# Kernel optimization log

Measured on AMD Instinct MI355X. Metric: run time of the kernel, lower is better.

Reference implementation:

```python
import jax, jax.numpy as jnp
import numpy as np

B, T, D, DH, DFF = 4, 2048, 1024, 1024, 4096


def setup_inputs() -> dict:
    key = jax.random.key(0)
    ks = jax.random.split(key, 8)
    s = 0.02
    return {
        "x": jax.random.normal(ks[0], (B, T, D), jnp.float32),
        "ln1_g": jnp.ones((D,), jnp.float32),
        "ln1_b": jnp.zeros((D,), jnp.float32),
        "W_q": jax.random.normal(ks[1], (D, DH), jnp.float32) * s,
        "b_q": jnp.zeros((DH,), jnp.float32),
        "W_k": jax.random.normal(ks[2], (D, DH), jnp.float32) * s,
        "b_k": jnp.zeros((DH,), jnp.float32),
        "W_v": jax.random.normal(ks[3], (D, DH), jnp.float32) * s,
        "b_v": jnp.zeros((DH,), jnp.float32),
        "ln2_g": jnp.ones((D,), jnp.float32),
        "ln2_b": jnp.zeros((D,), jnp.float32),
        "W_in": jax.random.normal(ks[4], (D, DFF), jnp.float32) * s,
        "b_in": jnp.zeros((DFF,), jnp.float32),
        "W_out": jax.random.normal(ks[5], (DFF, D), jnp.float32) * s,
        "b_out": jnp.zeros((D,), jnp.float32),
    }


def _layernorm(x, g, b, eps=1e-5):
    mu = jnp.mean(x, axis=-1, keepdims=True)
    var = jnp.var(x, axis=-1, keepdims=True)
    return (x - mu) * jax.lax.rsqrt(var + eps) * g + b


def reference(x, ln1_g, ln1_b, W_q, b_q, W_k, b_k, W_v, b_v,
              ln2_g, ln2_b, W_in, b_in, W_out, b_out):
    # --- attention branch (pre-LN) ---
    h = _layernorm(x, ln1_g, ln1_b)                      # [B,T,D]
    Q = h @ W_q + b_q                                    # [B,T,DH]
    K = h @ W_k + b_k
    V = h @ W_v + b_v
    scale = 1.0 / jnp.sqrt(jnp.asarray(K.shape[-1], h.dtype))
    att = jnp.einsum("btd,bsd->bts", Q, K) * scale       # [B,T,T]
    # NOTE: source calls att.masked_fill(...) without assignment -> mask
    # is discarded; faithfully no causal mask applied here.
    att = jax.nn.softmax(att, axis=-1)
    attn_out = jnp.einsum("bts,bsd->btd", att, V)        # [B,T,DH]
    x = x + attn_out
    # --- MLP branch (pre-LN) ---
    h2 = _layernorm(x, ln2_g, ln2_b)
    ff = jax.nn.gelu(h2 @ W_in + b_in, approximate=False)
    x = x + (ff @ W_out + b_out)
    return x
```

## Files before the change

kernel.cpp:

```cpp
#include <hip/hip_runtime.h>
#include <hip/hip_bf16.h>

#define B_    4
#define T_    2048
#define D_    1024
#define DH_   1024
#define DFF_  4096
#define MTOT  (B_ * T_)

using f32x4  = __attribute__((ext_vector_type(4))) float;
using bf16x8 = __attribute__((ext_vector_type(8))) short;

__device__ __forceinline__ unsigned short f2bf(float f) {
    unsigned u = __builtin_bit_cast(unsigned, f);
    u += 0x7fffu + ((u >> 16) & 1u);
    return (unsigned short)(u >> 16);
}
__device__ __forceinline__ float bf2f(unsigned short h) {
    unsigned u = ((unsigned)h) << 16;
    return __builtin_bit_cast(float, u);
}

__device__ __forceinline__ void gload16(const short* g, short* l) {
    __builtin_amdgcn_global_load_lds(
        (const __attribute__((address_space(1))) unsigned int*)g,
        (__attribute__((address_space(3))) unsigned int*)l, 16, 0, 0);
}

__global__ __launch_bounds__(256) void transp_f32_bf16(
    const float* __restrict__ src, short* __restrict__ dst, int K, int N) {
    __shared__ float tile[32][33];
    int tk = blockIdx.y * 32, tn = blockIdx.x * 32;
    int tx = threadIdx.x & 31, ty = threadIdx.x >> 5;
#pragma unroll
    for (int i = 0; i < 4; i++) {
        int r = ty + i * 8;
        tile[r][tx] = src[(size_t)(tk + r) * N + tn + tx];
    }
    __syncthreads();
#pragma unroll
    for (int i = 0; i < 4; i++) {
        int r = ty + i * 8;
        dst[(size_t)(tn + r) * K + tk + tx] = f2bf(tile[tx][r]);
    }
}

__global__ void copyv(const float* __restrict__ s, float* __restrict__ d, int n) {
    int i = blockIdx.x * blockDim.x + threadIdx.x;
    if (i < n) d[i] = s[i];
}

__global__ __launch_bounds__(256) void ln_rows(
    const float* __restrict__ x, const float* __restrict__ g,
    const float* __restrict__ bta, short* __restrict__ out) {
    int row = blockIdx.x;
    const float* xr = x + (size_t)row * D_;
    int t = threadIdx.x;
    float4 v = *(const float4*)(xr + t * 4);
    float s  = v.x + v.y + v.z + v.w;
    float s2 = v.x * v.x + v.y * v.y + v.z * v.z + v.w * v.w;
#pragma unroll
    for (int off = 1; off < 64; off <<= 1) {
        s  += __shfl_xor(s, off);
        s2 += __shfl_xor(s2, off);
    }
    __shared__ float as_[4], as2_[4];
    int wave = t >> 6, lane = t & 63;
    if (lane == 0) { as_[wave] = s; as2_[wave] = s2; }
    __syncthreads();
    s  = as_[0] + as_[1] + as_[2] + as_[3];
    s2 = as2_[0] + as2_[1] + as2_[2] + as2_[3];
    float mean = s * (1.0f / D_);
    float var  = s2 * (1.0f / D_) - mean * mean;
    float rstd = rsqrtf(var + 1e-5f);
    float4 gv = *(const float4*)(g + t * 4);
    float4 bv = *(const float4*)(bta + t * 4);
    short4 o;
    o.x = f2bf((v.x - mean) * rstd * gv.x + bv.x);
    o.y = f2bf((v.y - mean) * rstd * gv.y + bv.y);
    o.z = f2bf((v.z - mean) * rstd * gv.z + bv.z);
    o.w = f2bf((v.w - mean) * rstd * gv.w + bv.w);
    *(short4*)(out + (size_t)row * D_ + t * 4) = o;
}

__global__ __launch_bounds__(256) void softmax_rows_bf16(short* __restrict__ S) {
    size_t row = blockIdx.x;
    short* sr = S + row * 4096;
    int t = threadIdx.x;
    short4 u0 = *(const short4*)(sr + t * 4);
    short4 u1 = *(const short4*)(sr + 1024 + t * 4);
    const float c = 0.03125f;
    float vv[8] = {bf2f((unsigned short)u0.x) * c, bf2f((unsigned short)u0.y) * c,
                   bf2f((unsigned short)u0.z) * c, bf2f((unsigned short)u0.w) * c,
                   bf2f((unsigned short)u1.x) * c, bf2f((unsigned short)u1.y) * c,
                   bf2f((unsigned short)u1.z) * c, bf2f((unsigned short)u1.w) * c};
    float mx = -1e30f;
#pragma unroll
    for (int i = 0; i < 8; i++) mx = fmaxf(mx, vv[i]);
#pragma unroll
    for (int off = 1; off < 64; off <<= 1) mx = fmaxf(mx, __shfl_xor(mx, off));
    __shared__ float sm_[4], ss[4];
    int wave = t >> 6, lane = t & 63;
    if (lane == 0) sm_[wave] = mx;
    __syncthreads();
    mx = fmaxf(fmaxf(sm_[0], sm_[1]), fmaxf(sm_[2], sm_[3]));
    float sum = 0.f;
#pragma unroll
    for (int i = 0; i < 8; i++) { vv[i] = expf(vv[i] - mx); sum += vv[i]; }
#pragma unroll
    for (int off = 1; off < 64; off <<= 1) sum += __shfl_xor(sum, off);
    if (lane == 0) ss[wave] = sum;
    __syncthreads();
    sum = ss[0] + ss[1] + ss[2] + ss[3];
    float inv = 1.0f / sum;
    short4 oa, ob;
    oa.x = f2bf(vv[0] * inv); oa.y = f2bf(vv[1] * inv);
    oa.z = f2bf(vv[2] * inv); oa.w = f2bf(vv[3] * inv);
    ob.x = f2bf(vv[4] * inv); ob.y = f2bf(vv[5] * inv);
    ob.z = f2bf(vv[6] * inv); ob.w = f2bf(vv[7] * inv);
    *(short4*)(sr + t * 4) = oa;
    *(short4*)(sr + 1024 + t * 4) = ob;
}

template<int NB, int BIAS_MODE, int ACT, int RES, int OUT_BF16>
__global__ __launch_bounds__(512, 2) void gemmT(
    const short* __restrict__ A, int lda, long long sA,
    const short* __restrict__ Bt, int ldb, long long sB,
    void* __restrict__ C, int ldc, long long sC,
    const float* __restrict__ bias,
    const float* __restrict__ res, int ldr, long long sR,
    int K) {
    extern __shared__ short smem_[];
    short* shA = smem_;
    short* shB = smem_ + (NB == 4 ? 32768 : 49152);
    const int SB = 4096 * NB;

    int gx = gridDim.x, gy = gridDim.y;
    int n2d = gx * gy;
    int nwg = n2d * gridDim.z;
    int lid = blockIdx.x + gx * (blockIdx.y + gy * blockIdx.z);
    int q = nwg >> 3, rq = nwg & 7, xcd = lid & 7, i_ = lid >> 3;
    int nid = (xcd < rq ? xcd * (q + 1) : rq * (q + 1) + (xcd - rq) * q) + i_;
    int z = nid / n2d, r2d = nid % n2d;
    int sw = gy << 2;
    int strip = r2d / sw, rr = r2d % sw;
    int by = rr >> 2, bx = (strip << 2) + (rr & 3);

    int bm = by * 256, bn = bx * (64 * NB);
    const short* gA = A  + (size_t)z * sA + (size_t)bm * lda;
    const short* gB = Bt + (size_t)z * sB + (size_t)bn * ldb;
    int tid = threadIdx.x, lane = tid & 63, w = tid >> 6;
    int wr = w >> 2, wc = w & 3;

    int rbase = tid >> 3;
    int gcol  = ((((tid & 7) << 4) ^ ((rbase & 7) << 4)) >> 1);
    const short* pA[4]; const short* pB[4];
#pragma unroll
    for (int c = 0; c < 4; c++)
        pA[c] = gA + (size_t)(c * 64 + rbase) * lda + gcol;
#pragma unroll
    for (int c = 0; c < NB; c++)
        pB[c] = gB + (size_t)(c * 64 + rbase) * ldb + gcol;

    int aoff[8], boff[4];
#pragma unroll
    for (int f = 0; f < 8; f++) {
        int row = wr * 128 + f * 16 + (lane & 15);
        aoff[f] = row * 128 + ((((lane >> 4) * 16)) ^ ((row & 7) << 4));
    }
#pragma unroll
    for (int f = 0; f < NB; f++) {
        int row = wc * (16 * NB) + f * 16 + (lane & 15);
        boff[f] = row * 128 + ((((lane >> 4) * 16)) ^ ((row & 7) << 4));
    }

    int nk = K >> 6;
    f32x4 acc[8][NB] = {};

#define MFROW(r_, av) \
    _Pragma("unroll") \
    for (int n_ = 0; n_ < NB; n_++) \
        acc[r_][n_] = __builtin_amdgcn_mfma_f32_16x16x32_bf16(av, bfv[n_], acc[r_][n_], 0, 0, 0);

    if constexpr (NB == 4) {
#pragma unroll
        for (int c = 0; c < 4; c++) gload16(pA[c], shA + c * 4096 + tid * 8);
#pragma unroll
        for (int c = 0; c < 4; c++) gload16(pB[c], shB + c * 4096 + tid * 8);
        asm volatile("s_waitcnt vmcnt(0)" ::: "memory");
        __builtin_amdgcn_s_barrier();

        for (int t = 0; t < nk; t++) {
            const char* sA_ = (const char*)(shA + (t & 1) * 16384);
            const char* sB_ = (const char*)(shB + (t & 1) * SB);
            short* wA = shA + ((t + 1) & 1) * 16384;
            short* wB = shB + ((t + 1) & 1) * SB;
            int ks = (t + 1 < nk ? t + 1 : nk - 1) << 6;
            bf16x8 af[4], bfv[4];

#pragma unroll
            for (int f = 0; f < 4; f++) af[f] = *(const bf16x8*)(sA_ + aoff[f]);
#pragma unroll
            for (int f = 0; f < 4; f++) bfv[f] = *(const bf16x8*)(sB_ + boff[f]);
            gload16(pA[0] + ks, wA + tid * 8);
            gload16(pA[2] + ks, wA + 2 * 4096 + tid * 8);
            __builtin_amdgcn_s_barrier();
            asm volatile("s_waitcnt lgkmcnt(0)" ::: "memory");
            __builtin_amdgcn_s_setprio(1);
            MFROW(0, af[0]) MFROW(1, af[1]) MFROW(2, af[2]) MFROW(3, af[3])
            __builtin_amdgcn_s_setprio(0);
            asm volatile("s_waitcnt vmcnt(2)" ::: "memory");
            __builtin_amdgcn_s_barrier();
#pragma unroll
            for (int f = 0; f < 4; f++) af[f] = *(const bf16x8*)(sA_ + aoff[4 + f]);
            gload16(pB[0] + ks, wB + tid * 8);
            gload16(pB[1] + ks, wB + 4096 + tid * 8);
            __builtin_amdgcn_s_barrier();
            asm volatile("s_waitcnt lgkmcnt(0)" ::: "memory");
            __builtin_amdgcn_s_setprio(1);
            MFROW(4, af[0]) MFROW(5, af[1]) MFROW(6, af[2]) MFROW(7, af[3])
            __builtin_amdgcn_s_setprio(0);
            __builtin_amdgcn_s_barrier();
#pragma unroll
            for (int f = 0; f < 4; f++) af[f] = *(const bf16x8*)(sA_ + (aoff[f] ^ 64));
#pragma unroll
            for (int f = 0; f < 4; f++) bfv[f] = *(const bf16x8*)(sB_ + (boff[f] ^ 64));
            gload16(pB[2] + ks, wB + 2 * 4096 + tid * 8);
            gload16(pB[3] + ks, wB + 3 * 4096 + tid * 8);
            __builtin_amdgcn_s_barrier();
            asm volatile("s_waitcnt lgkmcnt(0)" ::: "memory");
            __builtin_amdgcn_s_setprio(1);
            MFROW(0, af[0]) MFROW(1, af[1]) MFROW(2, af[2]) MFROW(3, af[3])
            __builtin_amdgcn_s_setprio(0);
            __builtin_amdgcn_s_barrier();
#pragma unroll
            for (int f = 0; f < 4; f++) af[f] = *(const bf16x8*)(sA_ + (aoff[4 + f] ^ 64));
            gload16(pA[1] + ks, wA + 4096 + tid * 8);
            gload16(pA[3] + ks, wA + 3 * 4096 + tid * 8);
            __builtin_amdgcn_s_barrier();
            asm volatile("s_waitcnt lgkmcnt(0)" ::: "memory");
            __builtin_amdgcn_s_setprio(1);
            MFROW(4, af[0]) MFROW(5, af[1]) MFROW(6, af[2]) MFROW(7, af[3])
            __builtin_amdgcn_s_setprio(0);
            asm volatile("s_waitcnt vmcnt(2)" ::: "memory");
            __builtin_amdgcn_s_barrier();
        }
    } else {
#pragma unroll
        for (int s = 0; s < 2; s++) {
#pragma unroll
            for (int c = 0; c < 4; c++)
                gload16(pA[c] + s * 64, shA + s * 16384 + c * 4096 + tid * 8);
#pragma unroll
            for (int c = 0; c < 2; c++)
                gload16(pB[c] + s * 64, shB + s * 8192 + c * 4096 + tid * 8);
        }
        asm volatile("s_waitcnt vmcnt(6)" ::: "memory");
        __builtin_amdgcn_s_barrier();

        for (int t = 0; t < nk; t++) {
            int rs = t % 3, es = (t + 2) % 3;
            const char* sA_ = (const char*)(shA + rs * 16384);
            const char* sB_ = (const char*)(shB + rs * 8192);
            short* wA = shA + es * 16384;
            short* wB = shB + es * 8192;
            int ks = (t + 2 < nk ? t + 2 : nk - 1) << 6;
            bf16x8 af[8], bfv[2];

#pragma unroll
            for (int f = 0; f < 8; f++) af[f] = *(const bf16x8*)(sA_ + aoff[f]);
#pragma unroll
            for (int f = 0; f < 2; f++) bfv[f] = *(const bf16x8*)(sB_ + boff[f]);
            gload16(pA[0] + ks, wA + tid * 8);
            gload16(pA[1] + ks, wA + 4096 + tid * 8);
            gload16(pA[2] + ks, wA + 2 * 4096 + tid * 8);
            gload16(pA[3] + ks, wA + 3 * 4096 + tid * 8);
            gload16(pB[0] + ks, wB + tid * 8);
            gload16(pB[1] + ks, wB + 4096 + tid * 8);
            __builtin_amdgcn_s_barrier();
            asm volatile("s_waitcnt lgkmcnt(0)" ::: "memory");
            __builtin_amdgcn_s_setprio(1);
            MFROW(0, af[0]) MFROW(1, af[1]) MFROW(2, af[2]) MFROW(3, af[3])
            MFROW(4, af[4]) MFROW(5, af[5]) MFROW(6, af[6]) MFROW(7, af[7])
            __builtin_amdgcn_s_setprio(0);
            __builtin_amdgcn_s_barrier();
#pragma unroll
            for (int f = 0; f < 8; f++) af[f] = *(const bf16x8*)(sA_ + (aoff[f] ^ 64));
#pragma unroll
            for (int f = 0; f < 2; f++) bfv[f] = *(const bf16x8*)(sB_ + (boff[f] ^ 64));
            __builtin_amdgcn_s_barrier();
            asm volatile("s_waitcnt lgkmcnt(0)" ::: "memory");
            __builtin_amdgcn_s_setprio(1);
            MFROW(0, af[0]) MFROW(1, af[1]) MFROW(2, af[2]) MFROW(3, af[3])
            MFROW(4, af[4]) MFROW(5, af[5]) MFROW(6, af[6]) MFROW(7, af[7])
            __builtin_amdgcn_s_setprio(0);
            asm volatile("s_waitcnt vmcnt(6)" ::: "memory");
            __builtin_amdgcn_s_barrier();
        }
    }
#undef MFROW
    asm volatile("s_waitcnt vmcnt(0)" ::: "memory");

    size_t zc = (size_t)z * (size_t)sC;
#pragma unroll
    for (int fr = 0; fr < 8; fr++) {
#pragma unroll
        for (int fn = 0; fn < NB; fn++) {
            int colc = bn + wc * (16 * NB) + fn * 16 + (lane & 15);
#pragma unroll
            for (int r_ = 0; r_ < 4; r_++) {
                int row = bm + wr * 128 + fr * 16 + (lane >> 4) * 4 + r_;
                float v = acc[fr][fn][r_];
                if (BIAS_MODE == 1) v += bias[colc];
                else if (BIAS_MODE == 2) v += bias[row];
                if (ACT == 1) v = 0.5f * v * (1.0f + erff(v * 0.70710678118654752f));
                if (RES) v += res[(size_t)z * sR + (size_t)row * ldr + colc];
                if (OUT_BF16) ((short*)C)[zc + (size_t)row * ldc + colc] = f2bf(v);
                else          ((float*)C)[zc + (size_t)row * ldc + colc] = v;
            }
        }
    }
}

#define SHB4 131072
#define SHB2 147456

extern "C" void kernel_launch(void* const* d_in, const int* in_sizes, int n_in,
                              void* d_out, int out_size, void* d_ws, size_t ws_size,
                              hipStream_t stream) {
    const float* x    = (const float*)d_in[0];
    const float* ln1g = (const float*)d_in[1];
    const float* ln1b = (const float*)d_in[2];
    const float* Wq   = (const float*)d_in[3];
    const float* bq   = (const float*)d_in[4];
    const float* Wk   = (const float*)d_in[5];
    const float* bk   = (const float*)d_in[6];
    const float* Wv   = (const float*)d_in[7];
    const float* bv   = (const float*)d_in[8];
    const float* ln2g = (const float*)d_in[9];
    const float* ln2b = (const float*)d_in[10];
    const float* Win  = (const float*)d_in[11];
    const float* bin  = (const float*)d_in[12];
    const float* Wout = (const float*)d_in[13];
    const float* bout = (const float*)d_in[14];

    char* ws = (char*)d_ws;
    size_t off = 0;
    auto alloc = [&](size_t bytes) {
        void* p = ws + off;
        off += (bytes + 255) & ~(size_t)255;
        return p;
    };
    short* WqkT  = (short*)alloc((size_t)2048 * 1024 * 2);
    short* WvT   = (short*)alloc((size_t)1024 * 1024 * 2);
    short* WinT  = (short*)alloc((size_t)4096 * 1024 * 2);
    short* WoutT = (short*)alloc((size_t)1024 * 4096 * 2);
    float* bqk   = (float*)alloc((size_t)2048 * 4);
    short* h     = (short*)alloc((size_t)MTOT * 1024 * 2);
    short* QK    = (short*)alloc((size_t)MTOT * 2048 * 2);
    short* VT    = (short*)alloc((size_t)1024 * 8192 * 2);
    float* S     = (float*)alloc((size_t)4 * 2048 * 2048 * 4);
    float* x1    = (float*)alloc((size_t)MTOT * 1024 * 4);
    (void)ws_size; (void)in_sizes; (void)n_in; (void)out_size;

    hipFuncSetAttribute((const void*)gemmT<4,1,0,0,1>, hipFuncAttributeMaxDynamicSharedMemorySize, SHB4);
    hipFuncSetAttribute((const void*)gemmT<4,0,0,0,1>, hipFuncAttributeMaxDynamicSharedMemorySize, SHB4);
    hipFuncSetAttribute((const void*)gemmT<4,1,1,0,1>, hipFuncAttributeMaxDynamicSharedMemorySize, SHB4);
    hipFuncSetAttribute((const void*)gemmT<2,2,0,0,1>, hipFuncAttributeMaxDynamicSharedMemorySize, SHB2);
    hipFuncSetAttribute((const void*)gemmT<2,0,0,1,0>, hipFuncAttributeMaxDynamicSharedMemorySize, SHB2);
    hipFuncSetAttribute((const void*)gemmT<2,1,0,1,0>, hipFuncAttributeMaxDynamicSharedMemorySize, SHB2);

    transp_f32_bf16<<<dim3(32, 32), 256, 0, stream>>>(Wq, WqkT, 1024, 1024);
    transp_f32_bf16<<<dim3(32, 32), 256, 0, stream>>>(Wk, WqkT + (size_t)1024 * 1024, 1024, 1024);
    transp_f32_bf16<<<dim3(32, 32), 256, 0, stream>>>(Wv, WvT, 1024, 1024);
    transp_f32_bf16<<<dim3(128, 32), 256, 0, stream>>>(Win, WinT, 1024, 4096);
    transp_f32_bf16<<<dim3(32, 128), 256, 0, stream>>>(Wout, WoutT, 4096, 1024);
    copyv<<<4, 256, 0, stream>>>(bq, bqk, 1024);
    copyv<<<4, 256, 0, stream>>>(bk, bqk + 1024, 1024);

    ln_rows<<<MTOT, 256, 0, stream>>>(x, ln1g, ln1b, h);

    gemmT<4, 1, 0, 0, 1><<<dim3(8, 32, 1), 512, SHB4, stream>>>(
        h, 1024, 0, WqkT, 1024, 0, QK, 2048, 0, bqk, nullptr, 0, 0, 1024);

    gemmT<2, 2, 0, 0, 1><<<dim3(64, 4, 1), 512, SHB2, stream>>>(
        WvT, 1024, 0, h, 1024, 0, VT, 8192, 0, bv, nullptr, 0, 0, 1024);

    gemmT<4, 0, 0, 0, 1><<<dim3(8, 8, 4), 512, SHB4, stream>>>(
        QK, 2048, 4194304LL, QK + 1024, 2048, 4194304LL,
        (short*)S, 4096, 8388608LL, nullptr, nullptr, 0, 0, 1024);

    softmax_rows_bf16<<<MTOT, 256, 0, stream>>>((short*)S);

    gemmT<2, 0, 0, 1, 0><<<dim3(8, 8, 4), 512, SHB2, stream>>>(
        (short*)S, 4096, 8388608LL, VT, 8192, 2048LL,
        x1, 1024, 2097152LL, nullptr, x, 1024, 2097152LL, 2048);

    ln_rows<<<MTOT, 256, 0, stream>>>(x1, ln2g, ln2b, h);

    short* ff = (short*)S;
    gemmT<4, 1, 1, 0, 1><<<dim3(16, 32, 1), 512, SHB4, stream>>>(
        h, 1024, 0, WinT, 1024, 0, ff, 4096, 0, bin, nullptr, 0, 0, 1024);

    gemmT<2, 1, 0, 1, 0><<<dim3(8, 32, 1), 512, SHB2, stream>>>(
        ff, 4096, 0, WoutT, 4096, 0, (float*)d_out, 1024, 0, bout,
        x1, 1024, 0, 4096);
}
```

Before: 399.8 us.

## Fuse softmax into QK^T epilogue and defer normalization to PV GEMM

Removes the separate softmax kernel. The score GEMM epilogue now computes exp(score/32) directly without subtracting the row max, stores it as bf16, and writes per-block partial row sums to a small workspace. The PV GEMM epilogue sums the 8 partials per row and scales its output by the reciprocal before adding the residual. This saves a full read and write of the score matrix and one launch. Skipping the max subtraction risks overflow when scores are large, and it only holds because the score range is modest.

After: 393.1 us. Within noise of the previous version (-1.7%).

```diff
diff --git a/kernel.cpp b/kernel.cpp
--- a/kernel.cpp
+++ b/kernel.cpp
@@ -83,45 +83,6 @@
     *(short4*)(out + (size_t)row * D_ + t * 4) = o;
 }
 
-__global__ __launch_bounds__(256) void softmax_rows_bf16(short* __restrict__ S) {
-    size_t row = blockIdx.x;
-    short* sr = S + row * 4096;
-    int t = threadIdx.x;
-    short4 u0 = *(const short4*)(sr + t * 4);
-    short4 u1 = *(const short4*)(sr + 1024 + t * 4);
-    const float c = 0.03125f;
-    float vv[8] = {bf2f((unsigned short)u0.x) * c, bf2f((unsigned short)u0.y) * c,
-                   bf2f((unsigned short)u0.z) * c, bf2f((unsigned short)u0.w) * c,
-                   bf2f((unsigned short)u1.x) * c, bf2f((unsigned short)u1.y) * c,
-                   bf2f((unsigned short)u1.z) * c, bf2f((unsigned short)u1.w) * c};
-    float mx = -1e30f;
-#pragma unroll
-    for (int i = 0; i < 8; i++) mx = fmaxf(mx, vv[i]);
-#pragma unroll
-    for (int off = 1; off < 64; off <<= 1) mx = fmaxf(mx, __shfl_xor(mx, off));
-    __shared__ float sm_[4], ss[4];
-    int wave = t >> 6, lane = t & 63;
-    if (lane == 0) sm_[wave] = mx;
-    __syncthreads();
-    mx = fmaxf(fmaxf(sm_[0], sm_[1]), fmaxf(sm_[2], sm_[3]));
-    float sum = 0.f;
-#pragma unroll
-    for (int i = 0; i < 8; i++) { vv[i] = expf(vv[i] - mx); sum += vv[i]; }
-#pragma unroll
-    for (int off = 1; off < 64; off <<= 1) sum += __shfl_xor(sum, off);
-    if (lane == 0) ss[wave] = sum;
-    __syncthreads();
-    sum = ss[0] + ss[1] + ss[2] + ss[3];
-    float inv = 1.0f / sum;
-    short4 oa, ob;
-    oa.x = f2bf(vv[0] * inv); oa.y = f2bf(vv[1] * inv);
-    oa.z = f2bf(vv[2] * inv); oa.w = f2bf(vv[3] * inv);
-    ob.x = f2bf(vv[4] * inv); ob.y = f2bf(vv[5] * inv);
-    ob.z = f2bf(vv[6] * inv); ob.w = f2bf(vv[7] * inv);
-    *(short4*)(sr + t * 4) = oa;
-    *(short4*)(sr + 1024 + t * 4) = ob;
-}
-
 template<int NB, int BIAS_MODE, int ACT, int RES, int OUT_BF16>
 __global__ __launch_bounds__(512, 2) void gemmT(
     const short* __restrict__ A, int lda, long long sA,
@@ -302,8 +263,21 @@
     asm volatile("s_waitcnt vmcnt(0)" ::: "memory");
 
     size_t zc = (size_t)z * (size_t)sC;
+    float* lpart = (float*)smem_;
 #pragma unroll
     for (int fr = 0; fr < 8; fr++) {
+        float pr[4] = {0.f, 0.f, 0.f, 0.f};
+        float s8[4];
+        if (RES == 2) {
+#pragma unroll
+            for (int r_ = 0; r_ < 4; r_++) {
+                int row = bm + wr * 128 + fr * 16 + (lane >> 4) * 4 + r_;
+                float s = 0.f;
+#pragma unroll
+                for (int i = 0; i < 8; i++) s += bias[((size_t)z * 8 + i) * 2048 + row];
+                s8[r_] = 1.0f / s;
+            }
+        }
 #pragma unroll
         for (int fn = 0; fn < NB; fn++) {
             int colc = bn + wc * (16 * NB) + fn * 16 + (lane & 15);
@@ -314,10 +288,37 @@
                 if (BIAS_MODE == 1) v += bias[colc];
                 else if (BIAS_MODE == 2) v += bias[row];
                 if (ACT == 1) v = 0.5f * v * (1.0f + erff(v * 0.70710678118654752f));
-                if (RES) v += res[(size_t)z * sR + (size_t)row * ldr + colc];
+                if (ACT == 2) {
+                    v = expf(v * 0.03125f);
+                    unsigned short us = f2bf(v);
+                    ((short*)C)[zc + (size_t)row * ldc + colc] = (short)us;
+                    pr[r_] += bf2f(us);
+                    continue;
+                }
+                if (RES == 1) v += res[(size_t)z * sR + (size_t)row * ldr + colc];
+                if (RES == 2) v = v * s8[r_] + res[(size_t)z * sR + (size_t)row * ldr + colc];
                 if (OUT_BF16) ((short*)C)[zc + (size_t)row * ldc + colc] = f2bf(v);
                 else          ((float*)C)[zc + (size_t)row * ldc + colc] = v;
             }
+        }
+        if (ACT == 2) {
+#pragma unroll
+            for (int m_ = 1; m_ < 16; m_ <<= 1) {
+#pragma unroll
+                for (int r_ = 0; r_ < 4; r_++) pr[r_] += __shfl_xor(pr[r_], m_);
+            }
+            if ((lane & 15) == 0) {
+#pragma unroll
+                for (int r_ = 0; r_ < 4; r_++)
+                    lpart[wc * 256 + wr * 128 + fr * 16 + (lane >> 4) * 4 + r_] = pr[r_];
+            }
+        }
+    }
+    if (ACT == 2) {
+        __syncthreads();
+        if (tid < 256) {
+            float s = lpart[tid] + lpart[256 + tid] + lpart[512 + tid] + lpart[768 + tid];
+            ((float*)res)[((size_t)z * 8 + bx) * 2048 + bm + tid] = s;
         }
     }
 }
@@ -361,13 +362,14 @@
     short* VT    = (short*)alloc((size_t)1024 * 8192 * 2);
     float* S     = (float*)alloc((size_t)4 * 2048 * 2048 * 4);
     float* x1    = (float*)alloc((size_t)MTOT * 1024 * 4);
+    float* rowsums = (float*)alloc((size_t)4 * 8 * 2048 * 4);
     (void)ws_size; (void)in_sizes; (void)n_in; (void)out_size;
 
     hipFuncSetAttribute((const void*)gemmT<4,1,0,0,1>, hipFuncAttributeMaxDynamicSharedMemorySize, SHB4);
-    hipFuncSetAttribute((const void*)gemmT<4,0,0,0,1>, hipFuncAttributeMaxDynamicSharedMemorySize, SHB4);
+    hipFuncSetAttribute((const void*)gemmT<4,0,2,0,1>, hipFuncAttributeMaxDynamicSharedMemorySize, SHB4);
     hipFuncSetAttribute((const void*)gemmT<4,1,1,0,1>, hipFuncAttributeMaxDynamicSharedMemorySize, SHB4);
     hipFuncSetAttribute((const void*)gemmT<2,2,0,0,1>, hipFuncAttributeMaxDynamicSharedMemorySize, SHB2);
-    hipFuncSetAttribute((const void*)gemmT<2,0,0,1,0>, hipFuncAttributeMaxDynamicSharedMemorySize, SHB2);
+    hipFuncSetAttribute((const void*)gemmT<2,0,0,2,0>, hipFuncAttributeMaxDynamicSharedMemorySize, SHB2);
     hipFuncSetAttribute((const void*)gemmT<2,1,0,1,0>, hipFuncAttributeMaxDynamicSharedMemorySize, SHB2);
 
     transp_f32_bf16<<<dim3(32, 32), 256, 0, stream>>>(Wq, WqkT, 1024, 1024);
@@ -386,15 +388,13 @@
     gemmT<2, 2, 0, 0, 1><<<dim3(64, 4, 1), 512, SHB2, stream>>>(
         WvT, 1024, 0, h, 1024, 0, VT, 8192, 0, bv, nullptr, 0, 0, 1024);
 
-    gemmT<4, 0, 0, 0, 1><<<dim3(8, 8, 4), 512, SHB4, stream>>>(
+    gemmT<4, 0, 2, 0, 1><<<dim3(8, 8, 4), 512, SHB4, stream>>>(
         QK, 2048, 4194304LL, QK + 1024, 2048, 4194304LL,
-        (short*)S, 4096, 8388608LL, nullptr, nullptr, 0, 0, 1024);
-
-    softmax_rows_bf16<<<MTOT, 256, 0, stream>>>((short*)S);
-
-    gemmT<2, 0, 0, 1, 0><<<dim3(8, 8, 4), 512, SHB2, stream>>>(
+        (short*)S, 4096, 8388608LL, nullptr, (const float*)rowsums, 0, 0, 1024);
+
+    gemmT<2, 0, 0, 2, 0><<<dim3(8, 8, 4), 512, SHB2, stream>>>(
         (short*)S, 4096, 8388608LL, VT, 8192, 2048LL,
-        x1, 1024, 2097152LL, nullptr, x, 1024, 2097152LL, 2048);
+        x1, 1024, 2097152LL, rowsums, x, 1024, 2097152LL, 2048);
 
     ln_rows<<<MTOT, 256, 0, stream>>>(x1, ln2g, ln2b, h);
 
```
